# Kernel tuning notes

Hardware: AMD Instinct MI355X
Metric: run time of the kernel (lower is better)

Reference implementation:

```python
import jax, jax.numpy as jnp
import numpy as np


def _base_grid(B, H, W):
    xs = jnp.arange(W, dtype=jnp.float32)
    ys = jnp.arange(H, dtype=jnp.float32)
    gx, gy = jnp.meshgrid(xs, ys)  # [H,W] each, x varies along W
    return jnp.broadcast_to(jnp.stack([gx, gy], -1)[None], (B, H, W, 2))


def flow_to_grid(flow, accel=None):
    B, _, H, W = flow.shape
    v = 0.5 * flow
    if accel is not None:
        v = v + 0.25 * accel
    vgrid = _base_grid(B, H, W) + jnp.transpose(v, (0, 2, 3, 1))
    gx = 2.0 * vgrid[..., 0] / max(W - 1, 1) - 1.0
    gy = 2.0 * vgrid[..., 1] / max(H - 1, 1) - 1.0
    return jnp.stack([gx, gy], -1)  # [B,H,W,2]


def grid_sample_border(img, grid):
    # img [B,C,H,W], grid [B,Hg,Wg,2] normalized; bilinear, border pad, align_corners=True
    B, C, H, W = img.shape
    Hg, Wg = grid.shape[1], grid.shape[2]
    x = jnp.clip((grid[..., 0] + 1.0) * 0.5 * (W - 1), 0.0, W - 1)
    y = jnp.clip((grid[..., 1] + 1.0) * 0.5 * (H - 1), 0.0, H - 1)
    x0 = jnp.floor(x); y0 = jnp.floor(y)
    x1 = jnp.minimum(x0 + 1.0, W - 1); y1 = jnp.minimum(y0 + 1.0, H - 1)
    wx = (x - x0)[:, None]; wy = (y - y0)[:, None]  # [B,1,Hg,Wg]
    x0i, x1i, y0i, y1i = (a.astype(jnp.int32) for a in (x0, x1, y0, y1))
    flat = img.reshape(B, C, H * W)

    def gat(yi, xi):
        idx = jnp.broadcast_to((yi * W + xi).reshape(B, 1, Hg * Wg), (B, C, Hg * Wg))
        return jnp.take_along_axis(flat, idx, axis=2).reshape(B, C, Hg, Wg)

    v00, v01, v10, v11 = gat(y0i, x0i), gat(y0i, x1i), gat(y1i, x0i), gat(y1i, x1i)
    return v00 * (1 - wx) * (1 - wy) + v01 * wx * (1 - wy) + v10 * (1 - wx) * wy + v11 * wx * wy


def backward_warp(img, flow, accel=None):
    grid = flow_to_grid(flow, accel)
    warped = grid_sample_border(img, grid)
    valid = (jnp.abs(grid[..., 0]) <= 1.0) & (jnp.abs(grid[..., 1]) <= 1.0)
    return warped * valid[:, None].astype(img.dtype)


def local_kernel_warp(img, flow, kernel_params):
    B, C, H, W = img.shape
    k_row = jax.nn.softmax(kernel_params[:, :5], axis=1)   # [B,5,H,W]
    k_col = jax.nn.softmax(kernel_params[:, 5:10], axis=1)
    aniso = jax.nn.sigmoid(kernel_params[:, 10]) + 0.5     # [B,H,W]
    grid = flow_to_grid(flow)                               # [B,H,W,2]
    offsets = jnp.linspace(-2.0, 2.0, 5)
    a3 = aniso[..., None]                                   # [B,H,W,1]
    off_col = offsets.reshape(1, 1, 1, 5) * a3              # [B,H,W,5]
    off_row = offsets.reshape(1, 1, 1, 5) / a3
    zeros = jnp.zeros_like(off_row)
    grid_row = grid[:, :, :, None, :] + jnp.stack([off_row, zeros], -1) * (2.0 / W)
    samples_row = grid_sample_border(img, grid_row.reshape(B, H, W * 5, 2)).reshape(B, C, H, W, 5)
    img_row = jnp.einsum('bchwk,bkhw->bchw', samples_row, k_row)
    grid_base = flow_to_grid(jnp.zeros_like(flow))
    grid_col = grid_base[:, :, :, None, :] + jnp.stack([zeros, off_col], -1) * (2.0 / H)
    samples_col = grid_sample_border(img_row, grid_col.reshape(B, H, W * 5, 2)).reshape(B, C, H, W, 5)
    return jnp.einsum('bchwk,bkhw->bchw', samples_col, k_col)


def conv3x3(x, w, b):
    y = jax.lax.conv_general_dilated(x, w, (1, 1), 'SAME',
                                     dimension_numbers=('NCHW', 'OIHW', 'NCHW'))
    return y + b[None, :, None, None]


def reference(img, features, flow, kernel_params, w1, b1, w2, b2):
    B, _, H, W = img.shape
    Hf, Wf = features.shape[2], features.shape[3]
    warped_img = local_kernel_warp(img, flow, kernel_params)
    flow_scaled = jax.image.resize(flow, (B, 2, Hf, Wf), 'linear') * (Hf / H)
    warped_feat = backward_warp(features, flow_scaled)
    warped_img_down = jax.image.resize(warped_img, (B, 3, Hf, Wf), 'linear')
    x = jnp.concatenate([warped_feat, warped_img_down], axis=1)
    fused = conv3x3(jax.nn.relu(conv3x3(x, w1, b1)), w2, b2)
    return (warped_feat + fused, warped_img)


def setup_inputs() -> dict:
    key = jax.random.key(0)
    ks = jax.random.split(key, 6)
    B, H, W, Hf, Wf, Cf = 4, 512, 512, 256, 256, 96
    return {
        'img': jax.random.uniform(ks[0], (B, 3, H, W), jnp.float32),
        'features': jax.random.normal(ks[1], (B, Cf, Hf, Wf), jnp.float32),
        'flow': jax.random.normal(ks[2], (B, 2, H, W), jnp.float32) * 4.0,
        'kernel_params': jax.random.normal(ks[3], (B, 11, H, W), jnp.float32),
        'w1': jax.random.normal(ks[4], (Cf, Cf + 3, 3, 3), jnp.float32) * 0.02,
        'b1': jnp.zeros((Cf,), jnp.float32),
        'w2': jax.random.normal(ks[5], (Cf, Cf, 3, 3), jnp.float32) * 0.02,
        'b2': jnp.zeros((Cf,), jnp.float32),
    }
```

## Files before the change

### kernel.cpp

```cpp
#include <hip/hip_runtime.h>

#define NB 4
#define IH 512
#define IW 512
#define FH 256
#define FW 256
#define CF 96
#define C1 99
#define HWI (IH*IW)
#define HWF (FH*FW)
#define LDK 40

typedef short s8v __attribute__((ext_vector_type(8)));
typedef short s4v __attribute__((ext_vector_type(4)));
typedef float f4v __attribute__((ext_vector_type(4)));
typedef float f2v __attribute__((ext_vector_type(2), aligned(4)));

static __device__ __forceinline__ float sigmoidf_(float x) {
    return 1.0f / (1.0f + __expf(-x));
}
static __device__ __forceinline__ unsigned short f2bf(float f) {
    unsigned int u = __float_as_uint(f);
    unsigned int r = (u + 0x7fffu + ((u >> 16) & 1u)) >> 16;
    return (unsigned short)r;
}
static __device__ __forceinline__ float bf2f(short s) {
    unsigned int u = ((unsigned int)(unsigned short)s) << 16;
    return __uint_as_float(u);
}

__global__ __launch_bounds__(256)
void lkw_row_kernel(const float* __restrict__ img,
                    const float* __restrict__ flow,
                    const float* __restrict__ kp,
                    float* __restrict__ img_row) {
    int idx = blockIdx.x * blockDim.x + threadIdx.x;
    if (idx >= NB * HWI) return;
    int w = idx & (IW - 1);
    int h = (idx >> 9) & (IH - 1);
    int b = idx >> 18;

    const float* kpb = kp + (size_t)b * 11 * HWI + h * IW + w;
    float p[5];
    float m = -1e30f;
    #pragma unroll
    for (int k = 0; k < 5; k++) { p[k] = kpb[k * HWI]; m = fmaxf(m, p[k]); }
    float s = 0.f;
    #pragma unroll
    for (int k = 0; k < 5; k++) { p[k] = __expf(p[k] - m); s += p[k]; }
    float invs = 1.f / s;
    float a = sigmoidf_(kpb[10 * HWI]) + 0.5f;
    float inva = 1.f / a;

    float fx = flow[((size_t)b * 2 + 0) * HWI + h * IW + w];
    float fy = flow[((size_t)b * 2 + 1) * HWI + h * IW + w];

    float y = (float)h + 0.5f * fy;
    y = fminf(fmaxf(y, 0.f), (float)(IH - 1));
    float y0f = floorf(y);
    int y0 = (int)y0f;
    int y1 = min(y0 + 1, IH - 1);
    float wy = y - y0f;

    float xbase = (float)w + 0.5f * fx;
    const float sc = (float)(IW - 1) / (float)IW;

    const float* imb = img + (size_t)b * 3 * HWI;
    float acc0 = 0.f, acc1 = 0.f, acc2 = 0.f;
    #pragma unroll
    for (int k = 0; k < 5; k++) {
        float x = xbase + (float)(k - 2) * inva * sc;
        x = fminf(fmaxf(x, 0.f), (float)(IW - 1));
        float x0f = floorf(x);
        int x0 = (int)x0f;
        int x1 = min(x0 + 1, IW - 1);
        float wx = x - x0f;
        float wk = p[k] * invs;
        float w00 = (1.f - wx) * (1.f - wy) * wk;
        float w01 = wx * (1.f - wy) * wk;
        float w10 = (1.f - wx) * wy * wk;
        float w11 = wx * wy * wk;
        int i00 = y0 * IW + x0, i01 = y0 * IW + x1;
        int i10 = y1 * IW + x0, i11 = y1 * IW + x1;
        acc0 += w00 * imb[i00] + w01 * imb[i01] + w10 * imb[i10] + w11 * imb[i11];
        acc1 += w00 * imb[HWI + i00] + w01 * imb[HWI + i01] + w10 * imb[HWI + i10] + w11 * imb[HWI + i11];
        acc2 += w00 * imb[2 * HWI + i00] + w01 * imb[2 * HWI + i01] + w10 * imb[2 * HWI + i10] + w11 * imb[2 * HWI + i11];
    }
    img_row[(size_t)b * 3 * HWI + h * IW + w] = acc0;
    img_row[(size_t)b * 3 * HWI + HWI + h * IW + w] = acc1;
    img_row[(size_t)b * 3 * HWI + 2 * HWI + h * IW + w] = acc2;
}

__global__ __launch_bounds__(256)
void lkw_col_kernel(const float* __restrict__ img_row,
                    const float* __restrict__ kp,
                    float* __restrict__ out1) {
    int idx = blockIdx.x * blockDim.x + threadIdx.x;
    if (idx >= NB * HWI) return;
    int w = idx & (IW - 1);
    int h = (idx >> 9) & (IH - 1);
    int b = idx >> 18;

    const float* kpb = kp + (size_t)b * 11 * HWI + h * IW + w;
    float p[5];
    float m = -1e30f;
    #pragma unroll
    for (int k = 0; k < 5; k++) { p[k] = kpb[(5 + k) * HWI]; m = fmaxf(m, p[k]); }
    float s = 0.f;
    #pragma unroll
    for (int k = 0; k < 5; k++) { p[k] = __expf(p[k] - m); s += p[k]; }
    float invs = 1.f / s;
    float a = sigmoidf_(kpb[10 * HWI]) + 0.5f;

    const float sc = (float)(IH - 1) / (float)IH;
    const float* irb = img_row + (size_t)b * 3 * HWI;
    float acc0 = 0.f, acc1 = 0.f, acc2 = 0.f;
    #pragma unroll
    for (int k = 0; k < 5; k++) {
        float y = (float)h + (float)(k - 2) * a * sc;
        y = fminf(fmaxf(y, 0.f), (float)(IH - 1));
        float y0f = floorf(y);
        int y0 = (int)y0f;
        int y1 = min(y0 + 1, IH - 1);
        float wy = y - y0f;
        float wk = p[k] * invs;
        float w0 = (1.f - wy) * wk, w1 = wy * wk;
        int i0 = y0 * IW + w, i1 = y1 * IW + w;
        acc0 += w0 * irb[i0] + w1 * irb[i1];
        acc1 += w0 * irb[HWI + i0] + w1 * irb[HWI + i1];
        acc2 += w0 * irb[2 * HWI + i0] + w1 * irb[2 * HWI + i1];
    }
    out1[(size_t)b * 3 * HWI + h * IW + w] = acc0;
    out1[(size_t)b * 3 * HWI + HWI + h * IW + w] = acc1;
    out1[(size_t)b * 3 * HWI + 2 * HWI + h * IW + w] = acc2;
}

static __device__ __forceinline__ void ds_taps(int i, int n_in, int t[4], float wt[4]) {
    int n_out = n_in >> 1;
    if (i == 0) {
        t[0] = 0; t[1] = 0; t[2] = 1; t[3] = 2;
        wt[0] = 0.f; wt[1] = 3.f / 7.f; wt[2] = 3.f / 7.f; wt[3] = 1.f / 7.f;
    } else if (i == n_out - 1) {
        t[0] = n_in - 3; t[1] = n_in - 2; t[2] = n_in - 1; t[3] = n_in - 1;
        wt[0] = 1.f / 7.f; wt[1] = 3.f / 7.f; wt[2] = 3.f / 7.f; wt[3] = 0.f;
    } else {
        t[0] = 2 * i - 1; t[1] = 2 * i; t[2] = 2 * i + 1; t[3] = 2 * i + 2;
        wt[0] = 0.125f; wt[1] = 0.375f; wt[2] = 0.375f; wt[3] = 0.125f;
    }
}

__global__ __launch_bounds__(256)
void downsample2x_kernel(const float* __restrict__ src, float* __restrict__ dst,
                         int BC, float mul) {
    int idx = blockIdx.x * blockDim.x + threadIdx.x;
    if (idx >= BC * HWF) return;
    int j = idx & (FW - 1);
    int i = (idx >> 8) & (FH - 1);
    int bc = idx >> 16;

    int tx[4], ty[4];
    float wx[4], wy[4];
    ds_taps(j, IW, tx, wx);
    ds_taps(i, IH, ty, wy);
    const float* s = src + (size_t)bc * HWI;
    float acc = 0.f;
    #pragma unroll
    for (int a = 0; a < 4; a++) {
        if (wy[a] == 0.f) continue;
        const float* rp = s + (size_t)ty[a] * IW;
        float row = wx[0] * rp[tx[0]] + wx[1] * rp[tx[1]] + wx[2] * rp[tx[2]] + wx[3] * rp[tx[3]];
        acc += wy[a] * row;
    }
    dst[idx] = acc * mul;
}

__global__ __launch_bounds__(256)
void imgdown_cl_kernel(const float* __restrict__ out1, short* __restrict__ xin) {
    int idx = blockIdx.x * blockDim.x + threadIdx.x;
    if (idx >= NB * HWF) return;
    int j = idx & (FW - 1);
    int i = (idx >> 8) & (FH - 1);
    int b = idx >> 16;

    int tx[4], ty[4];
    float wx[4], wy[4];
    ds_taps(j, IW, tx, wx);
    ds_taps(i, IH, ty, wy);
    const float* s = out1 + (size_t)b * 3 * HWI;
    float acc[3] = {0.f, 0.f, 0.f};
    #pragma unroll
    for (int a = 0; a < 4; a++) {
        if (wy[a] == 0.f) continue;
        #pragma unroll
        for (int c = 0; c < 3; c++) {
            const float* rp = s + (size_t)c * HWI + (size_t)ty[a] * IW;
            float row = wx[0] * rp[tx[0]] + wx[1] * rp[tx[1]] + wx[2] * rp[tx[2]] + wx[3] * rp[tx[3]];
            acc[c] += wy[a] * row;
        }
    }
    short* dst = xin + ((size_t)(b * FH + i) * FW + j) * 128 + 96;
    s8v g0 = { (short)f2bf(acc[0]), (short)f2bf(acc[1]), (short)f2bf(acc[2]), 0, 0, 0, 0, 0 };
    s8v z  = { 0, 0, 0, 0, 0, 0, 0, 0 };
    *(s8v*)(dst)      = g0;
    *(s8v*)(dst + 8)  = z;
    *(s8v*)(dst + 16) = z;
    *(s8v*)(dst + 24) = z;
}

template <int BF>
__global__ __launch_bounds__(256)
void feat_cl_kernel(const float* __restrict__ feat, void* __restrict__ featT) {
    __shared__ float tile[64 * 97];
    int blk = blockIdx.x;
    int b = blk >> 10;
    int p0 = (blk & 1023) << 6;
    int t = threadIdx.x;
    {
        int px = t & 63, cq = t >> 6;
        const float* src = feat + (size_t)b * CF * HWF + p0 + px;
        #pragma unroll
        for (int k = 0; k < 24; k++) {
            int c = cq * 24 + k;
            tile[px * 97 + c] = src[(size_t)c * HWF];
        }
    }
    __syncthreads();
    int pxo = t >> 2, co = (t & 3) * 24;
    const float* trow = &tile[pxo * 97 + co];
    size_t obase = ((size_t)(b * HWF) + p0 + pxo) * 96 + co;
    if (BF) {
        short* dst = (short*)featT + obase;
        #pragma unroll
        for (int q = 0; q < 3; q++) {
            s8v pk;
            #pragma unroll
            for (int e = 0; e < 8; e++) pk[e] = (short)f2bf(trow[q * 8 + e]);
            *(s8v*)(dst + q * 8) = pk;
        }
    } else {
        float* dst = (float*)featT + obase;
        #pragma unroll
        for (int q = 0; q < 6; q++) {
            f4v vv = { trow[q * 4 + 0], trow[q * 4 + 1], trow[q * 4 + 2], trow[q * 4 + 3] };
            *(f4v*)(dst + q * 4) = vv;
        }
    }
}

template <int BF>
__global__ __launch_bounds__(256)
void warp_feat_cl2_kernel(const void* __restrict__ featT,
                          const float* __restrict__ flow_s,
                          float* __restrict__ wfeat,
                          short* __restrict__ xin) {
    int t = blockIdx.x * 256 + threadIdx.x;
    int g = t & 7;
    int pix = t >> 3;
    int j = pix & (FW - 1);
    int i = (pix >> 8) & (FH - 1);
    int b = pix >> 16;

    float fx = flow_s[((size_t)b * 2 + 0) * HWF + i * FW + j];
    float fy = flow_s[((size_t)b * 2 + 1) * HWF + i * FW + j];
    float u = (float)j + 0.5f * fx;
    float v = (float)i + 0.5f * fy;
    bool valid = (u >= 0.f) && (u <= (float)(FW - 1)) && (v >= 0.f) && (v <= (float)(FH - 1));
    float x = fminf(fmaxf(u, 0.f), (float)(FW - 1));
    float y = fminf(fmaxf(v, 0.f), (float)(FH - 1));
    int x0 = min((int)x, FW - 2);
    int y0 = min((int)y, FH - 2);
    float wxf = x - (float)x0, wyf = y - (float)y0;
    float w00 = (1.f - wxf) * (1.f - wyf), w01 = wxf * (1.f - wyf);
    float w10 = (1.f - wxf) * wyf, w11 = wxf * wyf;
    if (!valid) { w00 = w01 = w10 = w11 = 0.f; }

    size_t base = ((size_t)(b * HWF) + (size_t)y0 * FW + x0) * 96 + g * 12;
    float vals[12];
    if (BF) {
        const short* fp = (const short*)featT + base;
        #pragma unroll
        for (int q = 0; q < 3; q++) {
            s4v a0 = *(const s4v*)(fp + q * 4);
            s4v a1 = *(const s4v*)(fp + 96 + q * 4);
            s4v a2 = *(const s4v*)(fp + 96 * FW + q * 4);
            s4v a3 = *(const s4v*)(fp + 96 * FW + 96 + q * 4);
            #pragma unroll
            for (int e = 0; e < 4; e++)
                vals[q * 4 + e] = w00 * bf2f(a0[e]) + w01 * bf2f(a1[e])
                                + w10 * bf2f(a2[e]) + w11 * bf2f(a3[e]);
        }
    } else {
        const float* fp = (const float*)featT + base;
        #pragma unroll
        for (int q = 0; q < 3; q++) {
            f4v a0 = *(const f4v*)(fp + q * 4);
            f4v a1 = *(const f4v*)(fp + 96 + q * 4);
            f4v a2 = *(const f4v*)(fp + 96 * FW + q * 4);
            f4v a3 = *(const f4v*)(fp + 96 * FW + 96 + q * 4);
            #pragma unroll
            for (int e = 0; e < 4; e++)
                vals[q * 4 + e] = w00 * a0[e] + w01 * a1[e] + w10 * a2[e] + w11 * a3[e];
        }
    }

    float* ob = wfeat + ((size_t)b * CF + g * 12) * HWF + (size_t)i * FW + j;
    #pragma unroll
    for (int k = 0; k < 12; k++) ob[(size_t)k * HWF] = vals[k];

    short* xr = xin + (size_t)pix * 128 + g * 12;
    #pragma unroll
    for (int q2 = 0; q2 < 3; q2++) {
        s4v pk = { (short)f2bf(vals[q2 * 4 + 0]), (short)f2bf(vals[q2 * 4 + 1]),
                   (short)f2bf(vals[q2 * 4 + 2]), (short)f2bf(vals[q2 * 4 + 3]) };
        *(s4v*)(xr + q2 * 4) = pk;
    }
}

__global__ __launch_bounds__(256)
void warp_feat_cl_kernel(const float* __restrict__ feat,
                         const float* __restrict__ flow_s,
                         float* __restrict__ wfeat,
                         short* __restrict__ xin) {
    int t = blockIdx.x * 256 + threadIdx.x;
    int g = t & 7;
    int pix = t >> 3;
    int j = pix & (FW - 1);
    int i = (pix >> 8) & (FH - 1);
    int b = pix >> 16;

    float fx = flow_s[((size_t)b * 2 + 0) * HWF + i * FW + j];
    float fy = flow_s[((size_t)b * 2 + 1) * HWF + i * FW + j];
    float u = (float)j + 0.5f * fx;
    float v = (float)i + 0.5f * fy;
    bool valid = (u >= 0.f) && (u <= (float)(FW - 1)) && (v >= 0.f) && (v <= (float)(FH - 1));
    float x = fminf(fmaxf(u, 0.f), (float)(FW - 1));
    float y = fminf(fmaxf(v, 0.f), (float)(FH - 1));
    int x0 = min((int)x, FW - 2);
    int y0 = min((int)y, FH - 2);
    float wxf = x - (float)x0, wyf = y - (float)y0;
    float w00 = (1.f - wxf) * (1.f - wyf), w01 = wxf * (1.f - wyf);
    float w10 = (1.f - wxf) * wyf, w11 = wxf * wyf;
    if (!valid) { w00 = w01 = w10 = w11 = 0.f; }

    const float* fb = feat + ((size_t)b * CF + g * 12) * HWF + (size_t)y0 * FW + x0;
    float vals[12];
    #pragma unroll
    for (int k = 0; k < 12; k++) {
        const float* p = fb + (size_t)k * HWF;
        f2v r0 = *(const f2v*)p;
        f2v r1 = *(const f2v*)(p + FW);
        vals[k] = w00 * r0.x + w01 * r0.y + w10 * r1.x + w11 * r1.y;
    }

    float* ob = wfeat + ((size_t)b * CF + g * 12) * HWF + (size_t)i * FW + j;
    #pragma unroll
    for (int k = 0; k < 12; k++) ob[(size_t)k * HWF] = vals[k];

    short* xr = xin + (size_t)pix * 128 + g * 12;
    #pragma unroll
    for (int q2 = 0; q2 < 3; q2++) {
        s4v pk = { (short)f2bf(vals[q2 * 4 + 0]), (short)f2bf(vals[q2 * 4 + 1]),
                   (short)f2bf(vals[q2 * 4 + 2]), (short)f2bf(vals[q2 * 4 + 3]) };
        *(s4v*)(xr + q2 * 4) = pk;
    }
}

__global__ __launch_bounds__(256)
void cvt_w1_kernel(const float* __restrict__ w1, short* __restrict__ wA1) {
    int i = blockIdx.x * 256 + threadIdx.x;
    if (i >= 9 * 96 * 128) return;
    int ci = i & 127;
    int co = (i >> 7) % 96;
    int off = i / (96 * 128);
    float v = (ci < C1) ? w1[((size_t)co * C1 + ci) * 9 + off] : 0.f;
    wA1[i] = (short)f2bf(v);
}
__global__ __launch_bounds__(256)
void cvt_w2_kernel(const float* __restrict__ w2, short* __restrict__ wA2) {
    int i = blockIdx.x * 256 + threadIdx.x;
    if (i >= 9 * 96 * 96) return;
    int ci = i % 96;
    int co = (i / 96) % 96;
    int off = i / (96 * 96);
    wA2[i] = (short)f2bf(w2[((size_t)co * CF + ci) * 9 + off]);
}

template <int PASS>
__global__ __launch_bounds__(256)
void conv_mfma_kernel(const short* __restrict__ X,
                      const short* __restrict__ W,
                      const float* __restrict__ bias,
                      short* __restrict__ t1out,
                      float* __restrict__ out0) {
    constexpr int KSTR = (PASS == 1) ? 128 : 96;
    constexpr int KC = KSTR / 32;
    __shared__ short Als[96 * LDK];
    __shared__ short Bls[128 * LDK];

    const int bx = blockIdx.x;
    const int w0 = (bx & 1) * 128;
    const int h  = (bx >> 1) & (FH - 1);
    const int b  = bx >> 9;

    const int tid = threadIdx.x;
    const int lane = tid & 63;
    const int wv = tid >> 6;
    const int ln = lane & 15;
    const int q  = lane >> 4;

    f4v acc[6][2];
    #pragma unroll
    for (int mt = 0; mt < 6; mt++)
        #pragma unroll
        for (int nt = 0; nt < 2; nt++)
            acc[mt][nt] = (f4v){0.f, 0.f, 0.f, 0.f};

    const short* Xb = X + (size_t)(b * FH) * FW * KSTR;

    const int an = tid >> 1, ah = tid & 1;

    for (int off = 0; off < 9; ++off) {
        const int dy = off / 3 - 1, dx = off % 3 - 1;
        const int hy = h + dy;
        const bool hok = (hy >= 0) && (hy < FH);
        const short* Xrow = Xb + (size_t)hy * FW * KSTR;
        const short* Woff = W + (size_t)off * 96 * KSTR;
        const int wc = w0 + an + dx;
        const bool cok = hok && (wc >= 0) && (wc < FW);

        for (int kc = 0; kc < KC; ++kc) {
            const int ci0 = kc * 32;
            __syncthreads();
            if (tid < 192) {
                const short* srcA = Woff + (size_t)an * KSTR + ci0 + ah * 16;
                short* dstA = Als + an * LDK + ah * 16;
                *(float4*)dstA = *(const float4*)srcA;
                *(float4*)(dstA + 8) = *(const float4*)(srcA + 8);
            }
            {
                float4 vb0 = {0.f, 0.f, 0.f, 0.f};
                float4 vb1 = {0.f, 0.f, 0.f, 0.f};
                if (cok) {
                    const short* srcB = Xrow + (size_t)wc * KSTR + ci0 + ah * 16;
                    vb0 = *(const float4*)srcB;
                    vb1 = *(const float4*)(srcB + 8);
                }
                short* dstB = Bls + an * LDK + ah * 16;
                *(float4*)dstB = vb0;
                *(float4*)(dstB + 8) = vb1;
            }
            __syncthreads();
            s8v bfr0 = *(const s8v*)(Bls + (wv * 32 + ln) * LDK + q * 8);
            s8v bfr1 = *(const s8v*)(Bls + (wv * 32 + 16 + ln) * LDK + q * 8);
            #pragma unroll
            for (int mt = 0; mt < 6; ++mt) {
                s8v afr = *(const s8v*)(Als + (mt * 16 + ln) * LDK + q * 8);
                acc[mt][0] = __builtin_amdgcn_mfma_f32_16x16x32_bf16(afr, bfr0, acc[mt][0], 0, 0, 0);
                acc[mt][1] = __builtin_amdgcn_mfma_f32_16x16x32_bf16(afr, bfr1, acc[mt][1], 0, 0, 0);
            }
        }
    }

    if (PASS == 1) {
        const size_t rowbase = (size_t)(b * FH + h) * FW;
        #pragma unroll
        for (int nt = 0; nt < 2; ++nt) {
            int pos = w0 + wv * 32 + nt * 16 + ln;
            short* dst = t1out + (rowbase + pos) * CF;
            #pragma unroll
            for (int mt = 0; mt < 6; ++mt) {
                int co0 = mt * 16 + q * 4;
                s4v pk;
                #pragma unroll
                for (int r = 0; r < 4; ++r) {
                    float v = acc[mt][nt][r] + bias[co0 + r];
                    pk[r] = (short)f2bf(fmaxf(v, 0.f));
                }
                *(s4v*)(dst + co0) = pk;
            }
        }
    } else {
        #pragma unroll
        for (int nt = 0; nt < 2; ++nt) {
            int pos = w0 + wv * 32 + nt * 16 + ln;
            #pragma unroll
            for (int mt = 0; mt < 6; ++mt) {
                int co0 = mt * 16 + q * 4;
                #pragma unroll
                for (int r = 0; r < 4; ++r) {
                    size_t o = (size_t)(b * CF + co0 + r) * HWF + (size_t)h * FW + pos;
                    out0[o] += acc[mt][nt][r] + bias[co0 + r];
                }
            }
        }
    }
}

extern "C" void kernel_launch(void* const* d_in, const int* in_sizes, int n_in,
                              void* d_out, int out_size, void* d_ws, size_t ws_size,
                              hipStream_t stream) {
    const float* img  = (const float*)d_in[0];
    const float* feat = (const float*)d_in[1];
    const float* flow = (const float*)d_in[2];
    const float* kp   = (const float*)d_in[3];
    const float* w1   = (const float*)d_in[4];
    const float* b1   = (const float*)d_in[5];
    const float* w2   = (const float*)d_in[6];
    const float* b2   = (const float*)d_in[7];

    float* out0 = (float*)d_out;
    float* out1 = out0 + (size_t)NB * CF * HWF;

    char* wsb = (char*)d_ws;
    short* wA1 = (short*)wsb;
    short* wA2 = (short*)(wsb + 221184);
    short* xin = (short*)(wsb + 387072);
    const size_t off_after_xin = 387072 + 67108864;

    const size_t FEATT_F32 = (size_t)NB * HWF * 96 * 4;
    const size_t FEATT_BF16 = (size_t)NB * HWF * 96 * 2;
    const size_t FLOW_B = 2097152;
    const size_t need_f32 = off_after_xin + FLOW_B + FEATT_F32;
    const size_t need_b16 = off_after_xin + FLOW_B + FEATT_BF16;

    int n_img = NB * HWI;
    hipLaunchKernelGGL(cvt_w1_kernel, dim3((9 * 96 * 128 + 255) / 256), dim3(256), 0, stream, w1, wA1);
    hipLaunchKernelGGL(cvt_w2_kernel, dim3((9 * 96 * 96 + 255) / 256), dim3(256), 0, stream, w2, wA2);

    if (ws_size >= need_b16) {
        const bool f32ok = (ws_size >= need_f32);
        float* flow_s = (float*)(wsb + off_after_xin);
        char* region  = wsb + off_after_xin + FLOW_B;
        float* img_row = (float*)region;
        void*  featT   = (void*)region;
        short* t1cl    = (short*)region;

        hipLaunchKernelGGL(lkw_row_kernel, dim3((n_img + 255) / 256), dim3(256), 0, stream,
                           img, flow, kp, img_row);
        hipLaunchKernelGGL(lkw_col_kernel, dim3((n_img + 255) / 256), dim3(256), 0, stream,
                           img_row, kp, out1);
        hipLaunchKernelGGL(downsample2x_kernel, dim3((NB * 2 * HWF + 255) / 256), dim3(256), 0, stream,
                           flow, flow_s, NB * 2, 0.5f);
        hipLaunchKernelGGL(imgdown_cl_kernel, dim3((NB * HWF + 255) / 256), dim3(256), 0, stream,
                           out1, xin);
        if (f32ok) {
            hipLaunchKernelGGL((feat_cl_kernel<0>), dim3(NB * (HWF / 64)), dim3(256), 0, stream,
                               feat, featT);
            hipLaunchKernelGGL((warp_feat_cl2_kernel<0>), dim3(NB * HWF * 8 / 256), dim3(256), 0, stream,
                               featT, flow_s, out0, xin);
        } else {
            hipLaunchKernelGGL((feat_cl_kernel<1>), dim3(NB * (HWF / 64)), dim3(256), 0, stream,
                               feat, featT);
            hipLaunchKernelGGL((warp_feat_cl2_kernel<1>), dim3(NB * HWF * 8 / 256), dim3(256), 0, stream,
                               featT, flow_s, out0, xin);
        }
        hipLaunchKernelGGL((conv_mfma_kernel<1>), dim3(NB * FH * 2), dim3(256), 0, stream,
                           xin, wA1, b1, t1cl, (float*)nullptr);
        hipLaunchKernelGGL((conv_mfma_kernel<2>), dim3(NB * FH * 2), dim3(256), 0, stream,
                           t1cl, wA2, b2, (short*)nullptr, out0);
    } else {
        char* region = wsb + off_after_xin;
        short* t1cl    = (short*)region;
        float* img_row = (float*)region;
        float* flow_s  = (float*)(region + 16777216);

        hipLaunchKernelGGL(lkw_row_kernel, dim3((n_img + 255) / 256), dim3(256), 0, stream,
                           img, flow, kp, img_row);
        hipLaunchKernelGGL(lkw_col_kernel, dim3((n_img + 255) / 256), dim3(256), 0, stream,
                           img_row, kp, out1);
        hipLaunchKernelGGL(downsample2x_kernel, dim3((NB * 2 * HWF + 255) / 256), dim3(256), 0, stream,
                           flow, flow_s, NB * 2, 0.5f);
        hipLaunchKernelGGL(imgdown_cl_kernel, dim3((NB * HWF + 255) / 256), dim3(256), 0, stream,
                           out1, xin);
        hipLaunchKernelGGL(warp_feat_cl_kernel, dim3(NB * HWF * 8 / 256), dim3(256), 0, stream,
                           feat, flow_s, out0, xin);
        hipLaunchKernelGGL((conv_mfma_kernel<1>), dim3(NB * FH * 2), dim3(256), 0, stream,
                           xin, wA1, b1, t1cl, (float*)nullptr);
        hipLaunchKernelGGL((conv_mfma_kernel<2>), dim3(NB * FH * 2), dim3(256), 0, stream,
                           t1cl, wA2, b2, (short*)nullptr, out0);
    }
}
```

Before: 664.0 us.

## Reuse shifted input row across dx taps and prefetch next conv step into registers

The conv kernels now load one input row tile of 130 pixels per (kc, dy) step and reuse it for all three dx taps by offsetting the shared-memory read index. Weights are relaid as [kc][dy][dx][co][32] so all three dx weight slabs load in one step. The next step's global loads are issued into registers before the MFMAs run, overlapping memory with compute. This cuts barriers and redundant global loads by about three times, at the cost of larger shared memory (288+132 rows) and more registers.

```diff
diff --git a/kernel.cpp b/kernel.cpp
--- a/kernel.cpp
+++ b/kernel.cpp
@@ -368,34 +368,41 @@
 __global__ __launch_bounds__(256)
 void cvt_w1_kernel(const float* __restrict__ w1, short* __restrict__ wA1) {
     int i = blockIdx.x * 256 + threadIdx.x;
-    if (i >= 9 * 96 * 128) return;
-    int ci = i & 127;
-    int co = (i >> 7) % 96;
-    int off = i / (96 * 128);
-    float v = (ci < C1) ? w1[((size_t)co * C1 + ci) * 9 + off] : 0.f;
+    if (i >= 4 * 3 * 3 * 96 * 32) return;
+    int cl = i & 31;
+    int co = (i >> 5) % 96;
+    int rest = i / 3072;
+    int dx = rest % 3;
+    int dy = (rest / 3) % 3;
+    int kc = rest / 9;
+    int ci = kc * 32 + cl;
+    float v = (ci < C1) ? w1[((size_t)co * C1 + ci) * 9 + dy * 3 + dx] : 0.f;
     wA1[i] = (short)f2bf(v);
 }
 __global__ __launch_bounds__(256)
 void cvt_w2_kernel(const float* __restrict__ w2, short* __restrict__ wA2) {
     int i = blockIdx.x * 256 + threadIdx.x;
-    if (i >= 9 * 96 * 96) return;
-    int ci = i % 96;
-    int co = (i / 96) % 96;
-    int off = i / (96 * 96);
-    wA2[i] = (short)f2bf(w2[((size_t)co * CF + ci) * 9 + off]);
+    if (i >= 3 * 3 * 3 * 96 * 32) return;
+    int cl = i & 31;
+    int co = (i >> 5) % 96;
+    int rest = i / 3072;
+    int dx = rest % 3;
+    int dy = (rest / 3) % 3;
+    int kc = rest / 9;
+    wA2[i] = (short)f2bf(w2[((size_t)co * CF + kc * 32 + cl) * 9 + dy * 3 + dx]);
 }
 
 template <int PASS>
 __global__ __launch_bounds__(256)
-void conv_mfma_kernel(const short* __restrict__ X,
+void conv_mfma2_kernel(const short* __restrict__ X,
                       const short* __restrict__ W,
                       const float* __restrict__ bias,
                       short* __restrict__ t1out,
                       float* __restrict__ out0) {
     constexpr int KSTR = (PASS == 1) ? 128 : 96;
     constexpr int KC = KSTR / 32;
-    __shared__ short Als[96 * LDK];
-    __shared__ short Bls[128 * LDK];
+    __shared__ short Als[288 * LDK];
+    __shared__ short Bls[132 * LDK];
 
     const int bx = blockIdx.x;
     const int w0 = (bx & 1) * 128;
@@ -416,47 +423,79 @@
             acc[mt][nt] = (f4v){0.f, 0.f, 0.f, 0.f};
 
     const short* Xb = X + (size_t)(b * FH) * FW * KSTR;
-
-    const int an = tid >> 1, ah = tid & 1;
-
-    for (int off = 0; off < 9; ++off) {
-        const int dy = off / 3 - 1, dx = off % 3 - 1;
-        const int hy = h + dy;
-        const bool hok = (hy >= 0) && (hy < FH);
-        const short* Xrow = Xb + (size_t)hy * FW * KSTR;
-        const short* Woff = W + (size_t)off * 96 * KSTR;
-        const int wc = w0 + an + dx;
-        const bool cok = hok && (wc >= 0) && (wc < FW);
-
-        for (int kc = 0; kc < KC; ++kc) {
-            const int ci0 = kc * 32;
+    const int wp = w0 - 1 + tid;
+    const bool wok = (tid < 130) && (wp >= 0) && (wp < FW);
+
+    float4 pa[4], pa2[4], pb[4];
+
+    auto load_step = [&](int stepn, int kcn, int dyn) {
+        const short* srcA = W + ((size_t)stepn * 288 + tid) * 32;
+        pa[0] = *(const float4*)(srcA);
+        pa[1] = *(const float4*)(srcA + 8);
+        pa[2] = *(const float4*)(srcA + 16);
+        pa[3] = *(const float4*)(srcA + 24);
+        if (tid < 32) {
+            const short* srcA2 = srcA + 256 * 32;
+            pa2[0] = *(const float4*)(srcA2);
+            pa2[1] = *(const float4*)(srcA2 + 8);
+            pa2[2] = *(const float4*)(srcA2 + 16);
+            pa2[3] = *(const float4*)(srcA2 + 24);
+        }
+        int hy = h + dyn - 1;
+        if (wok && hy >= 0 && hy < FH) {
+            const short* srcB = Xb + ((size_t)hy * FW + wp) * KSTR + kcn * 32;
+            pb[0] = *(const float4*)(srcB);
+            pb[1] = *(const float4*)(srcB + 8);
+            pb[2] = *(const float4*)(srcB + 16);
+            pb[3] = *(const float4*)(srcB + 24);
+        } else {
+            pb[0] = pb[1] = pb[2] = pb[3] = (float4){0.f, 0.f, 0.f, 0.f};
+        }
+    };
+
+    load_step(0, 0, 0);
+
+    int step = 0;
+    for (int kc = 0; kc < KC; ++kc) {
+        for (int dy = 0; dy < 3; ++dy, ++step) {
             __syncthreads();
-            if (tid < 192) {
-                const short* srcA = Woff + (size_t)an * KSTR + ci0 + ah * 16;
-                short* dstA = Als + an * LDK + ah * 16;
-                *(float4*)dstA = *(const float4*)srcA;
-                *(float4*)(dstA + 8) = *(const float4*)(srcA + 8);
-            }
             {
-                float4 vb0 = {0.f, 0.f, 0.f, 0.f};
-                float4 vb1 = {0.f, 0.f, 0.f, 0.f};
-                if (cok) {
-                    const short* srcB = Xrow + (size_t)wc * KSTR + ci0 + ah * 16;
-                    vb0 = *(const float4*)srcB;
-                    vb1 = *(const float4*)(srcB + 8);
+                short* dA = Als + tid * LDK;
+                *(float4*)(dA)      = pa[0];
+                *(float4*)(dA + 8)  = pa[1];
+                *(float4*)(dA + 16) = pa[2];
+                *(float4*)(dA + 24) = pa[3];
+                if (tid < 32) {
+                    short* dA2 = Als + (256 + tid) * LDK;
+                    *(float4*)(dA2)      = pa2[0];
+                    *(float4*)(dA2 + 8)  = pa2[1];
+                    *(float4*)(dA2 + 16) = pa2[2];
+                    *(float4*)(dA2 + 24) = pa2[3];
                 }
-                short* dstB = Bls + an * LDK + ah * 16;
-                *(float4*)dstB = vb0;
-                *(float4*)(dstB + 8) = vb1;
+                if (tid < 130) {
+                    short* dB = Bls + tid * LDK;
+                    *(float4*)(dB)      = pb[0];
+                    *(float4*)(dB + 8)  = pb[1];
+                    *(float4*)(dB + 16) = pb[2];
+                    *(float4*)(dB + 24) = pb[3];
+                }
             }
             __syncthreads();
-            s8v bfr0 = *(const s8v*)(Bls + (wv * 32 + ln) * LDK + q * 8);
-            s8v bfr1 = *(const s8v*)(Bls + (wv * 32 + 16 + ln) * LDK + q * 8);
+            {
+                int ndy = dy + 1, nkc = kc;
+                if (ndy == 3) { ndy = 0; nkc++; }
+                if (nkc < KC) load_step(step + 1, nkc, ndy);
+            }
             #pragma unroll
-            for (int mt = 0; mt < 6; ++mt) {
-                s8v afr = *(const s8v*)(Als + (mt * 16 + ln) * LDK + q * 8);
-                acc[mt][0] = __builtin_amdgcn_mfma_f32_16x16x32_bf16(afr, bfr0, acc[mt][0], 0, 0, 0);
-                acc[mt][1] = __builtin_amdgcn_mfma_f32_16x16x32_bf16(afr, bfr1, acc[mt][1], 0, 0, 0);
+            for (int dx = 0; dx < 3; ++dx) {
+                s8v bfr0 = *(const s8v*)(Bls + (wv * 32 + ln + dx) * LDK + q * 8);
+                s8v bfr1 = *(const s8v*)(Bls + (wv * 32 + 16 + ln + dx) * LDK + q * 8);
+                #pragma unroll
+                for (int mt = 0; mt < 6; ++mt) {
+                    s8v afr = *(const s8v*)(Als + (dx * 96 + mt * 16 + ln) * LDK + q * 8);
+                    acc[mt][0] = __builtin_amdgcn_mfma_f32_16x16x32_bf16(afr, bfr0, acc[mt][0], 0, 0, 0);
+                    acc[mt][1] = __builtin_amdgcn_mfma_f32_16x16x32_bf16(afr, bfr1, acc[mt][1], 0, 0, 0);
+                }
             }
         }
     }
@@ -554,9 +593,9 @@
             hipLaunchKernelGGL((warp_feat_cl2_kernel<1>), dim3(NB * HWF * 8 / 256), dim3(256), 0, stream,
                                featT, flow_s, out0, xin);
         }
-        hipLaunchKernelGGL((conv_mfma_kernel<1>), dim3(NB * FH * 2), dim3(256), 0, stream,
+        hipLaunchKernelGGL((conv_mfma2_kernel<1>), dim3(NB * FH * 2), dim3(256), 0, stream,
                            xin, wA1, b1, t1cl, (float*)nullptr);
-        hipLaunchKernelGGL((conv_mfma_kernel<2>), dim3(NB * FH * 2), dim3(256), 0, stream,
+        hipLaunchKernelGGL((conv_mfma2_kernel<2>), dim3(NB * FH * 2), dim3(256), 0, stream,
                            t1cl, wA2, b2, (short*)nullptr, out0);
     } else {
         char* region = wsb + off_after_xin;
@@ -574,9 +613,9 @@
                            out1, xin);
         hipLaunchKernelGGL(warp_feat_cl_kernel, dim3(NB * HWF * 8 / 256), dim3(256), 0, stream,
                            feat, flow_s, out0, xin);
-        hipLaunchKernelGGL((conv_mfma_kernel<1>), dim3(NB * FH * 2), dim3(256), 0, stream,
+        hipLaunchKernelGGL((conv_mfma2_kernel<1>), dim3(NB * FH * 2), dim3(256), 0, stream,
                            xin, wA1, b1, t1cl, (float*)nullptr);
-        hipLaunchKernelGGL((conv_mfma_kernel<2>), dim3(NB * FH * 2), dim3(256), 0, stream,
+        hipLaunchKernelGGL((conv_mfma2_kernel<2>), dim3(NB * FH * 2), dim3(256), 0, stream,
                            t1cl, wA2, b2, (short*)nullptr, out0);
     }
 }
```

Result: slower. 781.6 us (+17.7%).
